# Kernel tuning notes

Measured on AMD Instinct MI355X. Metric: run time of the kernel, lower is better.

Reference implementation:

```python
import jax, jax.numpy as jnp
import numpy as np

# ---- module hyperparameters (mirror NDP defaults / init_kwargs) ----
ACTION_DIM = 16
NUM_BASIS = 4
NUM_ACTIONS = 50
BATCH = 32768
ALPHA_P = 1.0
ALPHA_U = 10.0
BETA = 2.5
DT = 0.01                      # ode_solver_dt
STEP_DELTA = 1.0 / NUM_ACTIONS # spacing of sample_times
N_SUB = int(round(STEP_DELTA / DT))  # integrator steps per save interval (=2)

RBF_CENTERS = jnp.exp(-ALPHA_P * jnp.linspace(0.0, 1.0, NUM_BASIS))
RBF_H = NUM_BASIS / RBF_CENTERS

# Tsitouras 5(4) Butcher tableau (same as diffrax.Tsit5); fixed step so only
# the 6 interior stages + 5th-order combination are needed (FSAL k7 unused).
A21 = 0.161
A31, A32 = -0.008480655492356989, 0.335480655492357
A41, A42, A43 = 2.8971530571054935, -6.359448489975075, 4.3622954328695815
A51, A52, A53, A54 = 5.325864828439257, -11.748883564062828, 7.4955393428898365, -0.09249506636175525
A61, A62, A63, A64, A65 = 5.86145544294642, -12.92096931784711, 8.159367898576159, -0.071584973281401, -0.028269050394068383
B1, B2, B3, B4, B5, B6 = 0.09646076681806523, 0.01, 0.4798896504144996, 1.379008574103742, -3.290069515436081, 2.324710524099774


def setup_inputs() -> dict:
    key = jax.random.key(0)
    k1, k2, k3 = jax.random.split(key, 3)
    return {
        "init_u_udot": 0.1 * jax.random.normal(k1, (BATCH, 2 * ACTION_DIM), jnp.float32),
        "rbf_weights": jax.random.normal(k2, (BATCH, ACTION_DIM * NUM_BASIS), jnp.float32),
        "goals": jax.random.normal(k3, (BATCH, ACTION_DIM), jnp.float32),
    }


def _ndp_flow(init_u_udot, rbf_weights, goals):
    """Batched fixed-step Tsit5 solve of the NDP ODE; returns u at sample_times."""
    B, A = init_u_udot.shape[0], ACTION_DIM
    u0s = init_u_udot[:, :A]
    W = rbf_weights.reshape(B, A, NUM_BASIS)
    gmu0 = goals - u0s                                      # (B, A), constant forcing scale
    y0 = jnp.concatenate([init_u_udot, jnp.ones((B, 1), init_u_udot.dtype)], axis=1)  # (B, 2A+1)

    def f(y):  # autonomous vector field, vectorized over batch
        u, ud, p = y[:, :A], y[:, A:2 * A], y[:, 2 * A:]    # p: (B,1)
        psi = jnp.exp(-RBF_H * (p - RBF_CENTERS) ** 2)      # (B, K)
        force = (jnp.einsum('bak,bk->ba', W, psi)
                 / jnp.sum(psi, axis=1, keepdims=True)) * p * gmu0
        udd = ALPHA_U * (BETA * (goals - u) - ud) + force
        return jnp.concatenate([ud, udd, -ALPHA_P * p], axis=1)

    h = DT

    def step(y, _):
        k1 = f(y)
        k2 = f(y + h * A21 * k1)
        k3 = f(y + h * (A31 * k1 + A32 * k2))
        k4 = f(y + h * (A41 * k1 + A42 * k2 + A43 * k3))
        k5 = f(y + h * (A51 * k1 + A52 * k2 + A53 * k3 + A54 * k4))
        k6 = f(y + h * (A61 * k1 + A62 * k2 + A63 * k3 + A64 * k4 + A65 * k5))
        yn = y + h * (B1 * k1 + B2 * k2 + B3 * k3 + B4 * k4 + B5 * k5 + B6 * k6)
        return yn, yn

    n_steps = (NUM_ACTIONS - 1) * N_SUB
    _, ys = jax.lax.scan(step, y0, None, length=n_steps)    # (steps, B, 2A+1)
    # sample_times[0] = 0 -> y0; later samples land exactly on every N_SUB-th step
    saved = jnp.concatenate([y0[None], ys[N_SUB - 1::N_SUB]], axis=0)  # (N, B, 2A+1)
    return jnp.transpose(saved[:, :, :A], (1, 0, 2))        # (B, N, A)


def reference(init_u_udot, rbf_weights, goals):
    return _ndp_flow(init_u_udot, rbf_weights, goals)
```

## Files before the change

### kernel.cpp

```cpp
#include <hip/hip_runtime.h>

namespace ct {

constexpr double H   = 0.01;
constexpr double A21 = 0.161;
constexpr double A31 = -0.008480655492356989, A32 = 0.335480655492357;
constexpr double A41 = 2.8971530571054935,  A42 = -6.359448489975075, A43 = 4.3622954328695815;
constexpr double A51 = 5.325864828439257,   A52 = -11.748883564062828, A53 = 7.4955393428898365, A54 = -0.09249506636175525;
constexpr double A61 = 5.86145544294642,    A62 = -12.92096931784711,  A63 = 8.159367898576159,  A64 = -0.071584973281401, A65 = -0.028269050394068383;
constexpr double B1 = 0.09646076681806523,  B2 = 0.01, B3 = 0.4798896504144996, B4 = 1.379008574103742, B5 = -3.290069515436081, B6 = 2.324710524099774;

constexpr double cexp(double x) {
    const double LN2 = 0.69314718055994530942;
    double t = x / LN2;
    int n = (int)(t >= 0.0 ? t + 0.5 : t - 0.5);
    double r = x - (double)n * LN2;
    double sum = 1.0, term = 1.0;
    for (int i = 1; i < 26; ++i) { term *= r / (double)i; sum += term; }
    if (n >= 0) { for (int i = 0; i <  n; ++i) sum *= 2.0; }
    else        { for (int i = 0; i < -n; ++i) sum *= 0.5; }
    return sum;
}

struct Pair { double u, d; };

constexpr Pair rk(double yu, double yd, const double* F) {
    double k1u = yd, k1d = -25.0*yu - 10.0*yd + F[0];
    double tu = yu + H*(A21*k1u), td = yd + H*(A21*k1d);
    double k2u = td, k2d = -25.0*tu - 10.0*td + F[1];
    tu = yu + H*(A31*k1u + A32*k2u); td = yd + H*(A31*k1d + A32*k2d);
    double k3u = td, k3d = -25.0*tu - 10.0*td + F[2];
    tu = yu + H*(A41*k1u + A42*k2u + A43*k3u);
    td = yd + H*(A41*k1d + A42*k2d + A43*k3d);
    double k4u = td, k4d = -25.0*tu - 10.0*td + F[3];
    tu = yu + H*(A51*k1u + A52*k2u + A53*k3u + A54*k4u);
    td = yd + H*(A51*k1d + A52*k2d + A53*k3d + A54*k4d);
    double k5u = td, k5d = -25.0*tu - 10.0*td + F[4];
    tu = yu + H*(A61*k1u + A62*k2u + A63*k3u + A64*k4u + A65*k5u);
    td = yd + H*(A61*k1d + A62*k2d + A63*k3d + A64*k4d + A65*k5d);
    double k6u = td, k6d = -25.0*tu - 10.0*td + F[5];
    double ou = yu + H*(B1*k1u + B2*k2u + B3*k3u + B4*k4u + B5*k5u + B6*k6u);
    double od = yd + H*(B1*k1d + B2*k2d + B3*k3d + B4*k4d + B5*k5d + B6*k6d);
    return {ou, od};
}

struct alignas(16) CoefTab { float c[50][8]; };

constexpr CoefTab make_coefs() {
    CoefTab T{};
    double vu[6] = {}, vd[6] = {};
    for (int i = 0; i < 6; ++i) {
        double F[6] = {0,0,0,0,0,0};
        F[i] = 1.0;
        Pair pr = rk(0.0, 0.0, F);
        vu[i] = pr.u; vd[i] = pr.d;
    }
    double Fz[6] = {0,0,0,0,0,0};
    Pair mc0 = rk(1.0, 0.0, Fz);
    Pair mc1 = rk(0.0, 1.0, Fz);
    double m00 = mc0.u, m10 = mc0.d, m01 = mc1.u, m11 = mc1.d;

    double gam[6] = {};
    double k1 = -1.0; gam[0] = 1.0;
    gam[1] = 1.0 + H*A21*k1;                                            double k2 = -gam[1];
    gam[2] = 1.0 + H*(A31*k1 + A32*k2);                                 double k3 = -gam[2];
    gam[3] = 1.0 + H*(A41*k1 + A42*k2 + A43*k3);                        double k4 = -gam[3];
    gam[4] = 1.0 + H*(A51*k1 + A52*k2 + A53*k3 + A54*k4);               double k5 = -gam[4];
    gam[5] = 1.0 + H*(A61*k1 + A62*k2 + A63*k3 + A64*k4 + A65*k5);      double k6 = -gam[5];
    double r = 1.0 + H*(B1*k1 + B2*k2 + B3*k3 + B4*k4 + B5*k5 + B6*k6);

    double C[4] = {}, Hh[4] = {};
    for (int k = 0; k < 4; ++k) { C[k] = cexp(-(double)k / 3.0); Hh[k] = 4.0 / C[k]; }

    double gvu = 0.0, gvd = 0.0;
    for (int i = 0; i < 6; ++i) { gvu += vu[i]; gvd += vd[i]; }
    gvu *= 25.0; gvd *= 25.0;

    double Su[7] = {1,0,0,0,0,0,0};
    double Sd[7] = {0,1,0,0,0,0,0};
    for (int j = 0; j < 7; ++j) T.c[0][j] = (float)Su[j];
    T.c[0][7] = 0.0f;

    double p = 1.0;
    int save = 1;
    for (int n = 0; n < 98; ++n) {
        double Qu[4] = {}, Qd[4] = {};
        for (int i = 0; i < 6; ++i) {
            double pi = gam[i] * p;
            double ps[4] = {}; double ss = 0.0;
            for (int k = 0; k < 4; ++k) {
                double d0 = pi - C[k];
                ps[k] = cexp(-Hh[k] * d0 * d0);
                ss += ps[k];
            }
            double sc = pi / ss;
            for (int k = 0; k < 4; ++k) {
                double sk = ps[k] * sc;
                Qu[k] += vu[i] * sk;
                Qd[k] += vd[i] * sk;
            }
        }
        double nu[7] = {}, nd[7] = {};
        for (int j = 0; j < 7; ++j) {
            nu[j] = m00*Su[j] + m01*Sd[j];
            nd[j] = m10*Su[j] + m11*Sd[j];
        }
        nu[2] += gvu; nd[2] += gvd;
        for (int k = 0; k < 4; ++k) { nu[3+k] += Qu[k]; nd[3+k] += Qd[k]; }
        for (int j = 0; j < 7; ++j) { Su[j] = nu[j]; Sd[j] = nd[j]; }
        p *= r;
        if (n & 1) {
            for (int j = 0; j < 7; ++j) T.c[save][j] = (float)Su[j];
            T.c[save][7] = 0.0f;
            ++save;
        }
    }
    return T;
}

}

constexpr ct::CoefTab h_coef = ct::make_coefs();
__constant__ ct::CoefTab g_coef = h_coef;

__global__ __launch_bounds__(256) void ndp_main(
    const float* __restrict__ init,
    const float* __restrict__ rbfw,
    const float* __restrict__ goals,
    float* __restrict__ out) {
    const int l  = threadIdx.x & 63;
    const int b  = blockIdx.x * 4 + (threadIdx.x >> 6);
    const int a4 = l & 3;
    const int r0 = l >> 2;

    const float4 u0  = *reinterpret_cast<const float4*>(&init[b * 32 + a4 * 4]);
    const float4 ud0 = *reinterpret_cast<const float4*>(&init[b * 32 + 16 + a4 * 4]);
    const float4 g4  = *reinterpret_cast<const float4*>(&goals[b * 16 + a4 * 4]);
    float4 gmu;
    gmu.x = g4.x - u0.x; gmu.y = g4.y - u0.y; gmu.z = g4.z - u0.z; gmu.w = g4.w - u0.w;

    const float4 wd0 = *reinterpret_cast<const float4*>(&rbfw[b * 64 + (4 * a4 + 0) * 4]);
    const float4 wd1 = *reinterpret_cast<const float4*>(&rbfw[b * 64 + (4 * a4 + 1) * 4]);
    const float4 wd2 = *reinterpret_cast<const float4*>(&rbfw[b * 64 + (4 * a4 + 2) * 4]);
    const float4 wd3 = *reinterpret_cast<const float4*>(&rbfw[b * 64 + (4 * a4 + 3) * 4]);
    float4 P0, P1, P2, P3;
    P0.x = gmu.x * wd0.x; P0.y = gmu.y * wd1.x; P0.z = gmu.z * wd2.x; P0.w = gmu.w * wd3.x;
    P1.x = gmu.x * wd0.y; P1.y = gmu.y * wd1.y; P1.z = gmu.z * wd2.y; P1.w = gmu.w * wd3.y;
    P2.x = gmu.x * wd0.z; P2.y = gmu.y * wd1.z; P2.z = gmu.z * wd2.z; P2.w = gmu.w * wd3.z;
    P3.x = gmu.x * wd0.w; P3.y = gmu.y * wd1.w; P3.z = gmu.z * wd2.w; P3.w = gmu.w * wd3.w;

    float* ob = out + (size_t)b * 800;
    #pragma unroll
    for (int j = 0; j < 4; ++j) {
        const int chunk = j * 64 + l;
        if (j < 3 || l < 8) {
            const int r = r0 + j * 16;
            const float4 c0 = *reinterpret_cast<const float4*>(&g_coef.c[r][0]);
            const float4 c1 = *reinterpret_cast<const float4*>(&g_coef.c[r][4]);
            float4 v;
            v.x = c0.x*u0.x + c0.y*ud0.x + c0.z*g4.x + c0.w*P0.x + c1.x*P1.x + c1.y*P2.x + c1.z*P3.x;
            v.y = c0.x*u0.y + c0.y*ud0.y + c0.z*g4.y + c0.w*P0.y + c1.x*P1.y + c1.y*P2.y + c1.z*P3.y;
            v.z = c0.x*u0.z + c0.y*ud0.z + c0.z*g4.z + c0.w*P0.z + c1.x*P1.z + c1.y*P2.z + c1.z*P3.z;
            v.w = c0.x*u0.w + c0.y*ud0.w + c0.z*g4.w + c0.w*P0.w + c1.x*P1.w + c1.y*P2.w + c1.z*P3.w;
            *reinterpret_cast<float4*>(ob + chunk * 4) = v;
        }
    }
}

extern "C" void kernel_launch(void* const* d_in, const int* in_sizes, int n_in,
                              void* d_out, int out_size, void* d_ws, size_t ws_size,
                              hipStream_t stream) {
    const float* init  = (const float*)d_in[0];
    const float* rbfw  = (const float*)d_in[1];
    const float* goals = (const float*)d_in[2];
    float* out = (float*)d_out;

    const int B = in_sizes[0] / 32;
    ndp_main<<<B / 4, 256, 0, stream>>>(init, rbfw, goals, out);
}
```

Before: 29.76 us.

## Process four batch rows per wave with prefetched inputs and hoisted coefficients

```diff
diff --git a/kernel.cpp b/kernel.cpp
--- a/kernel.cpp
+++ b/kernel.cpp
@@ -123,47 +123,72 @@
 constexpr ct::CoefTab h_coef = ct::make_coefs();
 __constant__ ct::CoefTab g_coef = h_coef;
 
+struct Feats { float4 u0, ud0, g4, w0, w1, w2, w3; };
+
+__device__ __forceinline__ Feats load_feats(const float* __restrict__ init,
+                                            const float* __restrict__ rbfw,
+                                            const float* __restrict__ goals,
+                                            int b, int a4) {
+    Feats f;
+    f.u0  = *reinterpret_cast<const float4*>(&init[b * 32 + a4 * 4]);
+    f.ud0 = *reinterpret_cast<const float4*>(&init[b * 32 + 16 + a4 * 4]);
+    f.g4  = *reinterpret_cast<const float4*>(&goals[b * 16 + a4 * 4]);
+    f.w0  = *reinterpret_cast<const float4*>(&rbfw[b * 64 + (4 * a4 + 0) * 4]);
+    f.w1  = *reinterpret_cast<const float4*>(&rbfw[b * 64 + (4 * a4 + 1) * 4]);
+    f.w2  = *reinterpret_cast<const float4*>(&rbfw[b * 64 + (4 * a4 + 2) * 4]);
+    f.w3  = *reinterpret_cast<const float4*>(&rbfw[b * 64 + (4 * a4 + 3) * 4]);
+    return f;
+}
+
 __global__ __launch_bounds__(256) void ndp_main(
     const float* __restrict__ init,
     const float* __restrict__ rbfw,
     const float* __restrict__ goals,
     float* __restrict__ out) {
     const int l  = threadIdx.x & 63;
-    const int b  = blockIdx.x * 4 + (threadIdx.x >> 6);
+    const int wv = blockIdx.x * 4 + (threadIdx.x >> 6);
     const int a4 = l & 3;
     const int r0 = l >> 2;
 
-    const float4 u0  = *reinterpret_cast<const float4*>(&init[b * 32 + a4 * 4]);
-    const float4 ud0 = *reinterpret_cast<const float4*>(&init[b * 32 + 16 + a4 * 4]);
-    const float4 g4  = *reinterpret_cast<const float4*>(&goals[b * 16 + a4 * 4]);
-    float4 gmu;
-    gmu.x = g4.x - u0.x; gmu.y = g4.y - u0.y; gmu.z = g4.z - u0.z; gmu.w = g4.w - u0.w;
-
-    const float4 wd0 = *reinterpret_cast<const float4*>(&rbfw[b * 64 + (4 * a4 + 0) * 4]);
-    const float4 wd1 = *reinterpret_cast<const float4*>(&rbfw[b * 64 + (4 * a4 + 1) * 4]);
-    const float4 wd2 = *reinterpret_cast<const float4*>(&rbfw[b * 64 + (4 * a4 + 2) * 4]);
-    const float4 wd3 = *reinterpret_cast<const float4*>(&rbfw[b * 64 + (4 * a4 + 3) * 4]);
-    float4 P0, P1, P2, P3;
-    P0.x = gmu.x * wd0.x; P0.y = gmu.y * wd1.x; P0.z = gmu.z * wd2.x; P0.w = gmu.w * wd3.x;
-    P1.x = gmu.x * wd0.y; P1.y = gmu.y * wd1.y; P1.z = gmu.z * wd2.y; P1.w = gmu.w * wd3.y;
-    P2.x = gmu.x * wd0.z; P2.y = gmu.y * wd1.z; P2.z = gmu.z * wd2.z; P2.w = gmu.w * wd3.z;
-    P3.x = gmu.x * wd0.w; P3.y = gmu.y * wd1.w; P3.z = gmu.z * wd2.w; P3.w = gmu.w * wd3.w;
-
-    float* ob = out + (size_t)b * 800;
+    float4 C0[4], C1[4];
     #pragma unroll
     for (int j = 0; j < 4; ++j) {
-        const int chunk = j * 64 + l;
-        if (j < 3 || l < 8) {
-            const int r = r0 + j * 16;
-            const float4 c0 = *reinterpret_cast<const float4*>(&g_coef.c[r][0]);
-            const float4 c1 = *reinterpret_cast<const float4*>(&g_coef.c[r][4]);
-            float4 v;
-            v.x = c0.x*u0.x + c0.y*ud0.x + c0.z*g4.x + c0.w*P0.x + c1.x*P1.x + c1.y*P2.x + c1.z*P3.x;
-            v.y = c0.x*u0.y + c0.y*ud0.y + c0.z*g4.y + c0.w*P0.y + c1.x*P1.y + c1.y*P2.y + c1.z*P3.y;
-            v.z = c0.x*u0.z + c0.y*ud0.z + c0.z*g4.z + c0.w*P0.z + c1.x*P1.z + c1.y*P2.z + c1.z*P3.z;
-            v.w = c0.x*u0.w + c0.y*ud0.w + c0.z*g4.w + c0.w*P0.w + c1.x*P1.w + c1.y*P2.w + c1.z*P3.w;
-            *reinterpret_cast<float4*>(ob + chunk * 4) = v;
-        }
+        const int r = (j == 3 && r0 >= 2) ? 0 : (r0 + j * 16);
+        C0[j] = *reinterpret_cast<const float4*>(&g_coef.c[r][0]);
+        C1[j] = *reinterpret_cast<const float4*>(&g_coef.c[r][4]);
+    }
+    const bool has4 = (r0 < 2);
+    const int b0 = wv * 4;
+
+    Feats f = load_feats(init, rbfw, goals, b0, a4);
+    #pragma unroll
+    for (int t = 0; t < 4; ++t) {
+        Feats fn;
+        if (t < 3) fn = load_feats(init, rbfw, goals, b0 + t + 1, a4);
+
+        float4 gmu;
+        gmu.x = f.g4.x - f.u0.x; gmu.y = f.g4.y - f.u0.y;
+        gmu.z = f.g4.z - f.u0.z; gmu.w = f.g4.w - f.u0.w;
+        float4 P0, P1, P2, P3;
+        P0.x = gmu.x * f.w0.x; P0.y = gmu.y * f.w1.x; P0.z = gmu.z * f.w2.x; P0.w = gmu.w * f.w3.x;
+        P1.x = gmu.x * f.w0.y; P1.y = gmu.y * f.w1.y; P1.z = gmu.z * f.w2.y; P1.w = gmu.w * f.w3.y;
+        P2.x = gmu.x * f.w0.z; P2.y = gmu.y * f.w1.z; P2.z = gmu.z * f.w2.z; P2.w = gmu.w * f.w3.z;
+        P3.x = gmu.x * f.w0.w; P3.y = gmu.y * f.w1.w; P3.z = gmu.z * f.w2.w; P3.w = gmu.w * f.w3.w;
+
+        float* ob = out + (size_t)(b0 + t) * 800;
+        #pragma unroll
+        for (int j = 0; j < 4; ++j) {
+            if (j < 3 || has4) {
+                const float4 c0 = C0[j], c1 = C1[j];
+                float4 v;
+                v.x = c0.x*f.u0.x + c0.y*f.ud0.x + c0.z*f.g4.x + c0.w*P0.x + c1.x*P1.x + c1.y*P2.x + c1.z*P3.x;
+                v.y = c0.x*f.u0.y + c0.y*f.ud0.y + c0.z*f.g4.y + c0.w*P0.y + c1.x*P1.y + c1.y*P2.y + c1.z*P3.y;
+                v.z = c0.x*f.u0.z + c0.y*f.ud0.z + c0.z*f.g4.z + c0.w*P0.z + c1.x*P1.z + c1.y*P2.z + c1.z*P3.z;
+                v.w = c0.x*f.u0.w + c0.y*f.ud0.w + c0.z*f.g4.w + c0.w*P0.w + c1.x*P1.w + c1.y*P2.w + c1.z*P3.w;
+                *reinterpret_cast<float4*>(ob + (j * 64 + l) * 4) = v;
+            }
+        }
+        f = fn;
     }
 }
 
@@ -176,5 +201,5 @@
     float* out = (float*)d_out;
 
     const int B = in_sizes[0] / 32;
-    ndp_main<<<B / 4, 256, 0, stream>>>(init, rbfw, goals, out);
-}
+    ndp_main<<<B / 16, 256, 0, stream>>>(init, rbfw, goals, out);
+}
```

New measurement: 24.70 us (median of 2 runs). -17.0%, faster.
